# Optimization experiments

Measured on AMD Instinct MI355X. Metric: run time of the kernel, lower is better.

## Reference

```python
import jax, jax.numpy as jnp
import numpy as np

M, N, C, D = 2, 8, 1024, 256  # n_routers, num_adapters, channel_dim, down_sample_size
B, S = 32, 512


def setup_inputs() -> dict:
    key = jax.random.key(0)
    k1, k2, k3, k4, k5 = jax.random.split(key, 5)
    x = jax.random.normal(k1, (B, S, C), dtype=jnp.float32)
    expert_index = jax.random.randint(k2, (M, B), 0, N, dtype=jnp.int32)
    down_w = jax.random.normal(k3, (M, N, C, D), dtype=jnp.float32) * 0.01
    down_b = jax.random.normal(k4, (M, N, D), dtype=jnp.float32) * 0.01
    up_w = jax.random.normal(k5, (M, N, D, C), dtype=jnp.float32) * 0.01
    return {"x": x, "expert_index": expert_index, "down_w": down_w,
            "down_b": down_b, "up_w": up_w}


def reference(x, expert_index, down_w, down_b, up_w):
    # Gather per-(router, batch-element) adapter weights along the adapter axis.
    idx = expert_index  # [M, B]
    bw_down = jnp.take_along_axis(down_w, idx[:, :, None, None], axis=1)  # [M, B, C, D]
    bb_down = jnp.take_along_axis(down_b, idx[:, :, None], axis=1)        # [M, B, D]
    bw_up = jnp.take_along_axis(up_w, idx[:, :, None, None], axis=1)      # [M, B, D, C]
    # z = swish(x @ W_down + b_down)  -> [M, B, S, D]
    z = jnp.einsum('bsc,mbcd->mbsd', x, bw_down) + bb_down[:, :, None, :]
    z = jax.nn.silu(z)
    # u = z @ W_up -> [M, B, S, C]
    u = jnp.einsum('mbsd,mbdc->mbsc', z, bw_up)
    return u
```

## Files before the change

### kernel.cpp

```cpp
#include <hip/hip_runtime.h>
#include <stdint.h>

typedef unsigned short u16;
typedef __bf16 bf16x8 __attribute__((ext_vector_type(8)));
typedef float f32x4 __attribute__((ext_vector_type(4)));

#define MM 2
#define NN 8
#define CC 1024
#define DD 256
#define BB 32
#define SS 512

__device__ __forceinline__ u16 f2bf(float f) {
  uint32_t u = __float_as_uint(f);
  u += 0x7FFFu + ((u >> 16) & 1u);
  return (u16)(u >> 16);
}

__device__ __forceinline__ void async16(const void* g, void* l) {
  __builtin_amdgcn_global_load_lds(
      (const __attribute__((address_space(1))) uint32_t*)g,
      (__attribute__((address_space(3))) uint32_t*)l, 16, 0, 0);
}

#define CVT_BLOCKS 16384
#define T_BLOCKS 4096
__global__ __launch_bounds__(256) void prep(
    const float* __restrict__ x, u16* __restrict__ xb,
    const float* __restrict__ dw, u16* __restrict__ wdT,
    const float* __restrict__ uw, u16* __restrict__ wuT) {
  const int bid = blockIdx.x;
  if (bid < CVT_BLOCKS) {
    int i = (bid * 256 + threadIdx.x) * 4;
    float4 v = *reinterpret_cast<const float4*>(x + i);
    u16 o[4] = {f2bf(v.x), f2bf(v.y), f2bf(v.z), f2bf(v.w)};
    *reinterpret_cast<uint2*>(xb + i) = *reinterpret_cast<const uint2*>(o);
    return;
  }
  __shared__ float tile[32][33];
  const float* src;
  u16* dst;
  int R, L, bx, by, slab;
  if (bid < CVT_BLOCKS + T_BLOCKS) {
    int t = bid - CVT_BLOCKS;
    slab = t >> 8;
    int t2 = t & 255;
    bx = t2 & 7;  by = t2 >> 3;
    R = CC; L = DD;
    src = dw; dst = wdT;
  } else {
    int t = bid - CVT_BLOCKS - T_BLOCKS;
    slab = t >> 8;
    int t2 = t & 255;
    bx = t2 & 31; by = t2 >> 5;
    R = DD; L = CC;
    src = uw; dst = wuT;
  }
  src += (size_t)slab * R * L;
  dst += (size_t)slab * R * L;
  const int c0 = bx * 32, r0 = by * 32;
  const int tx = threadIdx.x & 31, ty = threadIdx.x >> 5;
#pragma unroll
  for (int i = 0; i < 32; i += 8)
    tile[ty + i][tx] = src[(size_t)(r0 + ty + i) * L + c0 + tx];
  __syncthreads();
#pragma unroll
  for (int i = 0; i < 32; i += 8)
    dst[(size_t)(c0 + ty + i) * R + r0 + tx] = f2bf(tile[tx][ty + i]);
}

__global__ __launch_bounds__(512, 2) void fused_adapter(
    const u16* __restrict__ xb, const u16* __restrict__ wdT,
    const u16* __restrict__ wuT, const float* __restrict__ db,
    const int* __restrict__ eidx, float* __restrict__ out) {
  __shared__ __align__(16) u16 smA[2][128 * 32];
  __shared__ __align__(16) u16 smB[2][256 * 32];
  __shared__ __align__(16) u16 zl[8 * 128 * 32];

  const int pair = blockIdx.y;
  const int m = pair >> 5;
  const int b = pair & 31;
  const int e = eidx[pair];
  const int s0 = blockIdx.x * 128;

  const int tid = threadIdx.x;
  const int lane = tid & 63;
  const int wave = tid >> 6;
  const int quad = lane >> 4;
  const int l16 = lane & 15;

  const int srow = lane >> 2;
  const int kc = (lane & 3) * 8;

  const int wr = (wave >> 2) * 64;
  const int wc = (wave & 3) * 64;

  const u16* Ab = xb + ((size_t)b * SS + s0) * CC;
  const u16* Bd = wdT + (size_t)(m * NN + e) * DD * CC;
  const u16* Bu = wuT + (size_t)(m * NN + e) * CC * DD;

  const u16* gA = Ab + (size_t)(wave * 16 + srow) * CC + kc;
  const u16* gB0 = Bd + (size_t)(wave * 32 + srow) * CC + kc;
  const u16* gB1 = Bd + (size_t)(wave * 32 + 16 + srow) * CC + kc;
  const int lAo = wave * 16 * 32;
  const int lB0o = (wave * 32) * 32;
  const int lB1o = (wave * 32 + 16) * 32;

  f32x4 acc[4][4];
#pragma unroll
  for (int i = 0; i < 4; ++i)
#pragma unroll
    for (int j = 0; j < 4; ++j) acc[i][j] = (f32x4){0.f, 0.f, 0.f, 0.f};

  async16(gA, &smA[0][lAo]);
  async16(gB0, &smB[0][lB0o]);
  async16(gB1, &smB[0][lB1o]);
  __syncthreads();

  for (int kk = 0; kk < 32; ++kk) {
    const int cur = kk & 1, nxt = cur ^ 1;
    if (kk < 31) {
      const int ko = (kk + 1) * 32;
      async16(gA + ko, &smA[nxt][lAo]);
      async16(gB0 + ko, &smB[nxt][lB0o]);
      async16(gB1 + ko, &smB[nxt][lB1o]);
    } else {
      async16(Bu + (size_t)(wave * 32 + srow) * DD + kc, &smB[nxt][lB0o]);
      async16(Bu + (size_t)(wave * 32 + 16 + srow) * DD + kc, &smB[nxt][lB1o]);
    }
    bf16x8 af[4], bfr[4];
#pragma unroll
    for (int i = 0; i < 4; ++i)
      af[i] = *reinterpret_cast<const bf16x8*>(&smA[cur][(wr + i * 16 + l16) * 32 + quad * 8]);
#pragma unroll
    for (int j = 0; j < 4; ++j)
      bfr[j] = *reinterpret_cast<const bf16x8*>(&smB[cur][(wc + j * 16 + l16) * 32 + quad * 8]);
#pragma unroll
    for (int i = 0; i < 4; ++i)
#pragma unroll
      for (int j = 0; j < 4; ++j)
        acc[i][j] = __builtin_amdgcn_mfma_f32_16x16x32_bf16(af[i], bfr[j], acc[i][j], 0, 0, 0);
    __syncthreads();
  }

  const float* bias_p = db + (size_t)(m * NN + e) * DD;
#pragma unroll
  for (int j = 0; j < 4; ++j) {
    const int d = wc + j * 16 + l16;
    const float bias = bias_p[d];
    const int kt = d >> 5;
    const int kl = d & 31;
#pragma unroll
    for (int i = 0; i < 4; ++i) {
      const int zr = wr + i * 16 + quad * 4;
#pragma unroll
      for (int r = 0; r < 4; ++r) {
        float v = acc[i][j][r] + bias;
        v = v / (1.f + __expf(-v));
        zl[(kt * 128 + zr + r) * 32 + kl] = f2bf(v);
      }
    }
  }
  __syncthreads();

  float* ob = out + ((size_t)pair * SS + s0) * CC;

  for (int g = 0; g < 32; ++g) {
    const int cur = g & 1, nxt = cur ^ 1;
    const int ct = g >> 3;
    const int it = g & 7;
    if (g < 31) {
      const int g2 = g + 1;
      const int ct2 = g2 >> 3;
      const int ko2 = (g2 & 7) * 32;
      async16(Bu + (size_t)(ct2 * 256 + wave * 32 + srow) * DD + ko2 + kc, &smB[nxt][lB0o]);
      async16(Bu + (size_t)(ct2 * 256 + wave * 32 + 16 + srow) * DD + ko2 + kc, &smB[nxt][lB1o]);
    }
    if (it == 0) {
#pragma unroll
      for (int i = 0; i < 4; ++i)
#pragma unroll
        for (int j = 0; j < 4; ++j) acc[i][j] = (f32x4){0.f, 0.f, 0.f, 0.f};
    }
    bf16x8 af[4], bfr[4];
#pragma unroll
    for (int i = 0; i < 4; ++i)
      af[i] = *reinterpret_cast<const bf16x8*>(&zl[(it * 128 + wr + i * 16 + l16) * 32 + quad * 8]);
#pragma unroll
    for (int j = 0; j < 4; ++j)
      bfr[j] = *reinterpret_cast<const bf16x8*>(&smB[cur][(wc + j * 16 + l16) * 32 + quad * 8]);
#pragma unroll
    for (int i = 0; i < 4; ++i)
#pragma unroll
      for (int j = 0; j < 4; ++j)
        acc[i][j] = __builtin_amdgcn_mfma_f32_16x16x32_bf16(af[i], bfr[j], acc[i][j], 0, 0, 0);
    if (it == 7) {
#pragma unroll
      for (int j = 0; j < 4; ++j) {
        const int c = ct * 256 + wc + j * 16 + l16;
#pragma unroll
        for (int i = 0; i < 4; ++i) {
          const int sr = wr + i * 16 + quad * 4;
#pragma unroll
          for (int r = 0; r < 4; ++r)
            ob[(size_t)(sr + r) * CC + c] = acc[i][j][r];
        }
      }
    }
    __syncthreads();
  }
}

extern "C" void kernel_launch(void* const* d_in, const int* in_sizes, int n_in,
                              void* d_out, int out_size, void* d_ws, size_t ws_size,
                              hipStream_t stream) {
  const float* x  = (const float*)d_in[0];
  const int* eidx = (const int*)d_in[1];
  const float* dw = (const float*)d_in[2];
  const float* db = (const float*)d_in[3];
  const float* uw = (const float*)d_in[4];
  float* out = (float*)d_out;

  char* ws = (char*)d_ws;
  u16* xb  = (u16*)(ws);
  u16* wdT = (u16*)(ws + (size_t)32 * 1024 * 1024);
  u16* wuT = (u16*)(ws + (size_t)40 * 1024 * 1024);

  prep<<<dim3(CVT_BLOCKS + 2 * T_BLOCKS), dim3(256), 0, stream>>>(
      x, xb, dw, wdT, uw, wuT);
  fused_adapter<<<dim3(SS / 128, MM * BB), dim3(512), 0, stream>>>(
      xb, wdT, wuT, db, eidx, out);
}
```

Before: 277.5 us.

## Fuse x fp32-to-bf16 conversion into the adapter GEMM's A-tile loads

Drops the separate pass that converted x to bf16 in the workspace. The fused kernel now loads fp32 x directly into registers, converts it to bf16 and writes it to LDS after the MFMA step, software-pipelined one k-step ahead. This removes a 64MB read plus 32MB write-and-reread round trip. In exchange, each block reads the fp32 A-tile (twice the bytes), and x is read twice because each of the two routers reads it separately. The A loads also become synchronous register loads instead of async global-to-LDS copies.

```diff
diff --git a/kernel.cpp b/kernel.cpp
--- a/kernel.cpp
+++ b/kernel.cpp
@@ -18,39 +18,34 @@
   return (u16)(u >> 16);
 }
 
+__device__ __forceinline__ uint32_t pack2(float a, float b) {
+  return (uint32_t)f2bf(a) | ((uint32_t)f2bf(b) << 16);
+}
+
 __device__ __forceinline__ void async16(const void* g, void* l) {
   __builtin_amdgcn_global_load_lds(
       (const __attribute__((address_space(1))) uint32_t*)g,
       (__attribute__((address_space(3))) uint32_t*)l, 16, 0, 0);
 }
 
-#define CVT_BLOCKS 16384
 #define T_BLOCKS 4096
-__global__ __launch_bounds__(256) void prep(
-    const float* __restrict__ x, u16* __restrict__ xb,
+__global__ __launch_bounds__(256) void prep_w(
     const float* __restrict__ dw, u16* __restrict__ wdT,
     const float* __restrict__ uw, u16* __restrict__ wuT) {
   const int bid = blockIdx.x;
-  if (bid < CVT_BLOCKS) {
-    int i = (bid * 256 + threadIdx.x) * 4;
-    float4 v = *reinterpret_cast<const float4*>(x + i);
-    u16 o[4] = {f2bf(v.x), f2bf(v.y), f2bf(v.z), f2bf(v.w)};
-    *reinterpret_cast<uint2*>(xb + i) = *reinterpret_cast<const uint2*>(o);
-    return;
-  }
   __shared__ float tile[32][33];
   const float* src;
   u16* dst;
   int R, L, bx, by, slab;
-  if (bid < CVT_BLOCKS + T_BLOCKS) {
-    int t = bid - CVT_BLOCKS;
+  if (bid < T_BLOCKS) {
+    int t = bid;
     slab = t >> 8;
     int t2 = t & 255;
     bx = t2 & 7;  by = t2 >> 3;
     R = CC; L = DD;
     src = dw; dst = wdT;
   } else {
-    int t = bid - CVT_BLOCKS - T_BLOCKS;
+    int t = bid - T_BLOCKS;
     slab = t >> 8;
     int t2 = t & 255;
     bx = t2 & 31; by = t2 >> 5;
@@ -71,7 +66,7 @@
 }
 
 __global__ __launch_bounds__(512, 2) void fused_adapter(
-    const u16* __restrict__ xb, const u16* __restrict__ wdT,
+    const float* __restrict__ x, const u16* __restrict__ wdT,
     const u16* __restrict__ wuT, const float* __restrict__ db,
     const int* __restrict__ eidx, float* __restrict__ out) {
   __shared__ __align__(16) u16 smA[2][128 * 32];
@@ -96,14 +91,16 @@
   const int wr = (wave >> 2) * 64;
   const int wc = (wave & 3) * 64;
 
-  const u16* Ab = xb + ((size_t)b * SS + s0) * CC;
   const u16* Bd = wdT + (size_t)(m * NN + e) * DD * CC;
   const u16* Bu = wuT + (size_t)(m * NN + e) * CC * DD;
 
-  const u16* gA = Ab + (size_t)(wave * 16 + srow) * CC + kc;
+  const int arow = tid >> 2;
+  const int akseg = (tid & 3) * 8;
+  const float* gAx = x + ((size_t)b * SS + s0 + arow) * CC + akseg;
+  const int lAoff = arow * 32 + akseg;
+
   const u16* gB0 = Bd + (size_t)(wave * 32 + srow) * CC + kc;
   const u16* gB1 = Bd + (size_t)(wave * 32 + 16 + srow) * CC + kc;
-  const int lAo = wave * 16 * 32;
   const int lB0o = (wave * 32) * 32;
   const int lB1o = (wave * 32 + 16) * 32;
 
@@ -113,16 +110,24 @@
 #pragma unroll
     for (int j = 0; j < 4; ++j) acc[i][j] = (f32x4){0.f, 0.f, 0.f, 0.f};
 
-  async16(gA, &smA[0][lAo]);
+  {
+    float4 a0 = *reinterpret_cast<const float4*>(gAx + 0);
+    float4 a1 = *reinterpret_cast<const float4*>(gAx + 4);
+    *reinterpret_cast<uint4*>(&smA[0][lAoff]) =
+        make_uint4(pack2(a0.x, a0.y), pack2(a0.z, a0.w),
+                   pack2(a1.x, a1.y), pack2(a1.z, a1.w));
+  }
   async16(gB0, &smB[0][lB0o]);
   async16(gB1, &smB[0][lB1o]);
   __syncthreads();
 
   for (int kk = 0; kk < 32; ++kk) {
     const int cur = kk & 1, nxt = cur ^ 1;
+    float4 n0, n1;
     if (kk < 31) {
       const int ko = (kk + 1) * 32;
-      async16(gA + ko, &smA[nxt][lAo]);
+      n0 = *reinterpret_cast<const float4*>(gAx + ko + 0);
+      n1 = *reinterpret_cast<const float4*>(gAx + ko + 4);
       async16(gB0 + ko, &smB[nxt][lB0o]);
       async16(gB1 + ko, &smB[nxt][lB1o]);
     } else {
@@ -141,6 +146,11 @@
 #pragma unroll
       for (int j = 0; j < 4; ++j)
         acc[i][j] = __builtin_amdgcn_mfma_f32_16x16x32_bf16(af[i], bfr[j], acc[i][j], 0, 0, 0);
+    if (kk < 31) {
+      *reinterpret_cast<uint4*>(&smA[nxt][lAoff]) =
+          make_uint4(pack2(n0.x, n0.y), pack2(n0.z, n0.w),
+                     pack2(n1.x, n1.y), pack2(n1.z, n1.w));
+    }
     __syncthreads();
   }
 
@@ -167,15 +177,15 @@
   float* ob = out + ((size_t)pair * SS + s0) * CC;
 
   for (int g = 0; g < 32; ++g) {
-    const int cur = g & 1, nxt = cur ^ 1;
+    const int cur2 = g & 1, nxt2 = cur2 ^ 1;
     const int ct = g >> 3;
     const int it = g & 7;
     if (g < 31) {
       const int g2 = g + 1;
       const int ct2 = g2 >> 3;
       const int ko2 = (g2 & 7) * 32;
-      async16(Bu + (size_t)(ct2 * 256 + wave * 32 + srow) * DD + ko2 + kc, &smB[nxt][lB0o]);
-      async16(Bu + (size_t)(ct2 * 256 + wave * 32 + 16 + srow) * DD + ko2 + kc, &smB[nxt][lB1o]);
+      async16(Bu + (size_t)(ct2 * 256 + wave * 32 + srow) * DD + ko2 + kc, &smB[nxt2][lB0o]);
+      async16(Bu + (size_t)(ct2 * 256 + wave * 32 + 16 + srow) * DD + ko2 + kc, &smB[nxt2][lB1o]);
     }
     if (it == 0) {
 #pragma unroll
@@ -189,7 +199,7 @@
       af[i] = *reinterpret_cast<const bf16x8*>(&zl[(it * 128 + wr + i * 16 + l16) * 32 + quad * 8]);
 #pragma unroll
     for (int j = 0; j < 4; ++j)
-      bfr[j] = *reinterpret_cast<const bf16x8*>(&smB[cur][(wc + j * 16 + l16) * 32 + quad * 8]);
+      bfr[j] = *reinterpret_cast<const bf16x8*>(&smB[cur2][(wc + j * 16 + l16) * 32 + quad * 8]);
 #pragma unroll
     for (int i = 0; i < 4; ++i)
 #pragma unroll
@@ -223,12 +233,10 @@
   float* out = (float*)d_out;
 
   char* ws = (char*)d_ws;
-  u16* xb  = (u16*)(ws);
-  u16* wdT = (u16*)(ws + (size_t)32 * 1024 * 1024);
-  u16* wuT = (u16*)(ws + (size_t)40 * 1024 * 1024);
-
-  prep<<<dim3(CVT_BLOCKS + 2 * T_BLOCKS), dim3(256), 0, stream>>>(
-      x, xb, dw, wdT, uw, wuT);
+  u16* wdT = (u16*)(ws);
+  u16* wuT = (u16*)(ws + (size_t)8 * 1024 * 1024);
+
+  prep_w<<<dim3(2 * T_BLOCKS), dim3(256), 0, stream>>>(dw, wdT, uw, wuT);
   fused_adapter<<<dim3(SS / 128, MM * BB), dim3(512), 0, stream>>>(
-      xb, wdT, wuT, db, eidx, out);
-}
+      x, wdT, wuT, db, eidx, out);
+}
```

Measured after the change: 271.2 us. 1.02x faster.
